# Kernel optimization log

Measured on AMD Instinct MI355X. Metric: run time of the kernel, lower is better.

The kernel has to match this reference:

```python
import jax, jax.numpy as jnp
import numpy as np

NB, B, IN, HID = 8, 256, 512, 512
G = 4 * HID
WB, IB, ABNM = 8, 8, 8
NL = 0.05


def quant(x, bits, r):
    # QuantFunc.forward: scale, clamp to (-1+1/step, 1-1/step), round to step grid, rescale
    step = 2.0 ** (bits - 1)
    x01 = jnp.clip(x / r, -1.0 + 1.0 / step, 1.0 - 1.0 / step)
    return jnp.round(x01 * step) / step * r


def pact(x, a):
    # pact_a_bmm vectorized over the block dim: sign(x)*0.5*(|x| - ||x|-a| + a)
    a3 = a[:, None, None]
    return jnp.sign(x) * 0.5 * (jnp.abs(x) - jnp.abs(jnp.abs(x) - a3) + a3)


def custom_mm(inp, w, b, nw, nb):
    # CustomMM_bmm.forward: quantize weights/bias (range 1.0), add scaled noise, bmm
    wq = quant(w, WB, 1.0)
    bq = quant(b, WB, 1.0)
    out = jnp.einsum('bni,bio->bno', inp, wq + nw * jnp.max(w) * NL)
    return out + bq + nb * jnp.max(b) * NL


def setup_inputs():
    key = jax.random.key(0)
    ks = jax.random.split(key, 11)
    inp = {
        'input': jax.random.normal(ks[0], (B, IN), jnp.float32),
        'hx': jax.random.normal(ks[1], (NB, B, HID), jnp.float32),
        'cx': jax.random.normal(ks[2], (NB, B, HID), jnp.float32),
        'weight_ih': jax.random.normal(ks[3], (NB, IN, G), jnp.float32),
        'weight_hh': jax.random.normal(ks[4], (NB, HID, G), jnp.float32),
        'bias_ih': jax.random.normal(ks[5], (NB, 1, G), jnp.float32),
        'bias_hh': jax.random.normal(ks[6], (NB, 1, G), jnp.float32),
        'noise_wih': jax.random.normal(ks[7], (NB, IN, G), jnp.float32),
        'noise_whh': jax.random.normal(ks[8], (NB, HID, G), jnp.float32),
        'noise_bih': jax.random.normal(ks[9], (NB, 1, G), jnp.float32),
        'noise_bhh': jax.random.normal(ks[10], (NB, 1, G), jnp.float32),
        'a1': jnp.full((NB,), 128.0, jnp.float32),
        'a3': jnp.ones((NB,), jnp.float32),
        'a4': jnp.ones((NB,), jnp.float32),
        'a5': jnp.ones((NB,), jnp.float32),
        'a6': jnp.ones((NB,), jnp.float32),
        'a7': jnp.full((NB,), 4.0, jnp.float32),
        'a8': jnp.ones((NB,), jnp.float32),
        'a9': jnp.full((NB,), 4.0, jnp.float32),
        'a10': jnp.ones((NB,), jnp.float32),
        'a11': jnp.full((NB,), 4.0, jnp.float32),
    }
    return inp


def reference(input, hx, cx, weight_ih, weight_hh, bias_ih, bias_hh,
              noise_wih, noise_whh, noise_bih, noise_bhh,
              a1, a3, a4, a5, a6, a7, a8, a9, a10, a11):
    xr = jnp.broadcast_to(input[None], (NB,) + input.shape)  # input.repeat(n_blocks,1,1)
    xq = quant(pact(xr, a1), IB, a1[:, None, None])
    gates = custom_mm(xq, weight_ih, bias_ih, noise_wih, noise_bih) \
          + custom_mm(hx, weight_hh, bias_hh, noise_whh, noise_bhh)
    i, j, f, o = jnp.split(gates, 4, axis=2)
    qp = lambda x, a: quant(pact(x, a), ABNM, a[:, None, None])
    fg = qp(jax.nn.sigmoid(f), a3)
    ig = qp(jax.nn.sigmoid(i), a4)
    act = qp(jnp.tanh(j), a5)
    og = qp(jax.nn.sigmoid(o), a6)
    gated = qp(cx * fg, a7)
    actin = qp(ig * act, a8)
    new_c = qp(gated + actin, a9)
    actc = qp(jnp.tanh(new_c), a10)
    new_h = qp(actc * og, a11)
    return new_h, new_c
```

## Files before the change

### kernel.cpp

```cpp
#include <hip/hip_runtime.h>
#include <hip/hip_bf16.h>

#define NBATCH 8
#define BROWS 256
#define KDIM 512
#define HIDD 512
#define GDIM 2048
#define KSTEP 32
#define NIT (KDIM / KSTEP)

typedef float f32x4 __attribute__((ext_vector_type(4)));
typedef __bf16 bf16x8 __attribute__((ext_vector_type(8)));

__device__ __forceinline__ unsigned fenc(float f) {
    unsigned u = __float_as_uint(f);
    return (u & 0x80000000u) ? ~u : (u | 0x80000000u);
}
__device__ __forceinline__ float fdec(unsigned e) {
    unsigned u = (e & 0x80000000u) ? (e & 0x7fffffffu) : ~e;
    return __uint_as_float(u);
}
__device__ __forceinline__ unsigned umaxu(unsigned a, unsigned b) { return a > b ? a : b; }

__device__ __forceinline__ float qpact(float x, float a) {
    float ax = fabsf(x);
    float p  = copysignf(0.5f * (ax - fabsf(ax - a) + a), x);
    float x01 = p / a;
    x01 = fminf(fmaxf(x01, -0.9921875f), 0.9921875f);
    return (rintf(x01 * 128.f) * 0.0078125f) * a;
}
__device__ __forceinline__ float q1(float x) {
    float x01 = fminf(fmaxf(x, -0.9921875f), 0.9921875f);
    return rintf(x01 * 128.f) * 0.0078125f;
}
__device__ __forceinline__ float sigmf(float x) { return 1.0f / (1.0f + expf(-x)); }

__global__ void k_init(unsigned* m) { if (threadIdx.x < 4) m[threadIdx.x] = 0u; }

__global__ void k_max(const float* __restrict__ w_ih, const float* __restrict__ w_hh,
                      const float* __restrict__ b_ih, const float* __restrict__ b_hh,
                      unsigned* __restrict__ omax) {
    int which = blockIdx.y;
    const float* src = which == 0 ? w_ih : which == 1 ? w_hh : which == 2 ? b_ih : b_hh;
    int n4 = (which < 2 ? NBATCH * KDIM * GDIM : NBATCH * GDIM) >> 2;
    unsigned best = 0u;
    int stride = gridDim.x * blockDim.x;
    for (int i = blockIdx.x * blockDim.x + threadIdx.x; i < n4; i += stride) {
        float4 v = ((const float4*)src)[i];
        best = umaxu(best, fenc(v.x)); best = umaxu(best, fenc(v.y));
        best = umaxu(best, fenc(v.z)); best = umaxu(best, fenc(v.w));
    }
    #pragma unroll
    for (int off = 32; off > 0; off >>= 1)
        best = umaxu(best, (unsigned)__shfl_down((int)best, off, 64));
    __shared__ unsigned red[4];
    int lane = threadIdx.x & 63, wv = threadIdx.x >> 6;
    if (lane == 0) red[wv] = best;
    __syncthreads();
    if (threadIdx.x == 0) {
        unsigned b2 = umaxu(umaxu(red[0], red[1]), umaxu(red[2], red[3]));
        atomicMax(&omax[which], b2);
    }
}

__global__ void k_prep(const float* __restrict__ input, const float* __restrict__ hx,
                       const float* __restrict__ bih, const float* __restrict__ bhh,
                       const float* __restrict__ nbih, const float* __restrict__ nbhh,
                       const float* __restrict__ a1, const unsigned* __restrict__ maxes,
                       __hip_bfloat16* __restrict__ xqh, __hip_bfloat16* __restrict__ hxh,
                       __hip_bfloat16* __restrict__ hxl, float* __restrict__ bias_comb) {
    const int NX = NBATCH * BROWS * KDIM;
    const int NH = NBATCH * BROWS * HIDD;
    const int NBC = NBATCH * GDIM;
    int total = NX + NH + NBC;
    int stride = gridDim.x * blockDim.x;
    for (int i = blockIdx.x * blockDim.x + threadIdx.x; i < total; i += stride) {
        if (i < NX) {
            int nb = i >> 17;
            int rem = i & 131071;
            float v = qpact(input[rem], a1[nb]);
            xqh[i] = __float2bfloat16(v);
        } else if (i < NX + NH) {
            int j = i - NX;
            float h = hx[j];
            __hip_bfloat16 hi = __float2bfloat16(h);
            hxh[j] = hi;
            hxl[j] = __float2bfloat16(h - __bfloat162float(hi));
        } else {
            int j = i - NX - NH;
            float mb_ih = fdec(maxes[2]);
            float mb_hh = fdec(maxes[3]);
            bias_comb[j] = q1(bih[j]) + (nbih[j] * mb_ih) * 0.05f
                         + q1(bhh[j]) + (nbhh[j] * mb_hh) * 0.05f;
        }
    }
}

__global__ __launch_bounds__(512, 2) void k_gemm(
    const float* __restrict__ w_ih, const float* __restrict__ w_hh,
    const float* __restrict__ n_ih, const float* __restrict__ n_hh,
    const __hip_bfloat16* __restrict__ xqh, const __hip_bfloat16* __restrict__ hxh,
    const __hip_bfloat16* __restrict__ hxl,
    const float* __restrict__ bias_comb, const float* __restrict__ cx,
    const float* __restrict__ a3, const float* __restrict__ a4, const float* __restrict__ a5,
    const float* __restrict__ a6, const float* __restrict__ a7, const float* __restrict__ a8,
    const float* __restrict__ a9, const float* __restrict__ a10, const float* __restrict__ a11,
    const unsigned* __restrict__ maxes,
    float* __restrict__ out_h, float* __restrict__ out_c)
{
    __shared__ __hip_bfloat16 Bsm[2][4][64][40];

    int tid = threadIdx.x;
    int lane = tid & 63, wv = tid >> 6;
    int nb = blockIdx.x & 7;
    int cb = blockIdx.x >> 3;

    const float* wih_b = w_ih + nb * KDIM * GDIM;
    const float* whh_b = w_hh + nb * KDIM * GDIM;
    const float* nih_b = n_ih + nb * KDIM * GDIM;
    const float* nhh_b = n_hh + nb * KDIM * GDIM;
    const __hip_bfloat16* xq_b = xqh + nb * BROWS * KDIM;
    const __hip_bfloat16* hh_b = hxh + nb * BROWS * KDIM;
    const __hip_bfloat16* hl_b = hxl + nb * BROWS * KDIM;

    float c_ih = fdec(maxes[0]);
    float c_hh = fdec(maxes[1]);

    f32x4 acc[2][4] = {};

    int lh = lane & 15;
    int lk = (lane >> 4) << 3;
    int m0 = wv << 5;

    int sn0 = (tid & 15) << 2;
    int sk  = tid >> 4;
    int scol = ((sn0 >> 4) << 9) + (cb << 4) + (sn0 & 15);
    int sbase = sk * GDIM + scol;

    f32x4 rw1a, rz1a, rw2a, rz2a;
    f32x4 rw1b, rz1b, rw2b, rz2b;
    bf16x8 axv[2], ahv[2], alv[2];

#define STAGE(RW1, RZ1, RW2, RZ2, K0) {            \
    int gx = sbase + (K0) * GDIM;                  \
    RW1 = *(const f32x4*)(wih_b + gx);             \
    RZ1 = *(const f32x4*)(nih_b + gx);             \
    RW2 = *(const f32x4*)(whh_b + gx);             \
    RZ2 = *(const f32x4*)(nhh_b + gx); }

#define ALOAD(K0) {                                \
    _Pragma("unroll")                              \
    for (int mf = 0; mf < 2; ++mf) {               \
        int aoff = (m0 + (mf << 4) + lh) * KDIM + (K0) + lk; \
        axv[mf] = *(const bf16x8*)(xq_b + aoff);   \
        ahv[mf] = *(const bf16x8*)(hh_b + aoff);   \
        alv[mf] = *(const bf16x8*)(hl_b + aoff); } }

#define CVT(P, RW1, RZ1, RW2, RZ2) {               \
    _Pragma("unroll")                              \
    for (int j = 0; j < 4; ++j) {                  \
        float w1 = RW1[j], z1 = RZ1[j];            \
        float wq1 = rintf(fminf(fmaxf(w1, -0.9921875f), 0.9921875f) * 128.f) * 0.0078125f; \
        float e1 = wq1 + (z1 * c_ih) * 0.05f;      \
        __hip_bfloat16 h1 = __float2bfloat16(e1);  \
        Bsm[P][0][sn0 + j][sk] = h1;               \
        Bsm[P][1][sn0 + j][sk] = __float2bfloat16(e1 - __bfloat162float(h1)); \
        float w2 = RW2[j], z2 = RZ2[j];            \
        float wq2 = rintf(fminf(fmaxf(w2, -0.9921875f), 0.9921875f) * 128.f) * 0.0078125f; \
        float e2 = wq2 + (z2 * c_hh) * 0.05f;      \
        __hip_bfloat16 h2 = __float2bfloat16(e2);  \
        Bsm[P][2][sn0 + j][sk] = h2;               \
        Bsm[P][3][sn0 + j][sk] = __float2bfloat16(e2 - __bfloat162float(h2)); \
    } }

#define COMPUTE(P) {                               \
    _Pragma("unroll")                              \
    for (int nf = 0; nf < 4; ++nf) {               \
        int n = (nf << 4) + lh;                    \
        bf16x8 b0 = *(const bf16x8*)&Bsm[P][0][n][lk]; \
        bf16x8 b1 = *(const bf16x8*)&Bsm[P][1][n][lk]; \
        bf16x8 b2 = *(const bf16x8*)&Bsm[P][2][n][lk]; \
        bf16x8 b3 = *(const bf16x8*)&Bsm[P][3][n][lk]; \
        _Pragma("unroll")                          \
        for (int mf = 0; mf < 2; ++mf) {           \
            acc[mf][nf] = __builtin_amdgcn_mfma_f32_16x16x32_bf16(axv[mf], b0, acc[mf][nf], 0, 0, 0); \
            acc[mf][nf] = __builtin_amdgcn_mfma_f32_16x16x32_bf16(axv[mf], b1, acc[mf][nf], 0, 0, 0); \
            acc[mf][nf] = __builtin_amdgcn_mfma_f32_16x16x32_bf16(ahv[mf], b2, acc[mf][nf], 0, 0, 0); \
            acc[mf][nf] = __builtin_amdgcn_mfma_f32_16x16x32_bf16(ahv[mf], b3, acc[mf][nf], 0, 0, 0); \
            acc[mf][nf] = __builtin_amdgcn_mfma_f32_16x16x32_bf16(alv[mf], b2, acc[mf][nf], 0, 0, 0); \
        } \
    } }

    STAGE(rw1a, rz1a, rw2a, rz2a, 0);
    STAGE(rw1b, rz1b, rw2b, rz2b, KSTEP);

    for (int it = 0; it < NIT; it += 2) {
        ALOAD(it * KSTEP);
        CVT(0, rw1a, rz1a, rw2a, rz2a);
        if (it + 2 < NIT) STAGE(rw1a, rz1a, rw2a, rz2a, (it + 2) * KSTEP);
        __syncthreads();
        COMPUTE(0);
        ALOAD((it + 1) * KSTEP);
        CVT(1, rw1b, rz1b, rw2b, rz2b);
        if (it + 3 < NIT) STAGE(rw1b, rz1b, rw2b, rz2b, (it + 3) * KSTEP);
        __syncthreads();
        COMPUTE(1);
    }

    int hcol = (cb << 4) + lh;
    float A3 = a3[nb], A4 = a4[nb], A5 = a5[nb], A6 = a6[nb], A7 = a7[nb];
    float A8 = a8[nb], A9 = a9[nb], A10 = a10[nb], A11 = a11[nb];
    float bc_i = bias_comb[nb * GDIM + hcol];
    float bc_j = bias_comb[nb * GDIM + 512 + hcol];
    float bc_f = bias_comb[nb * GDIM + 1024 + hcol];
    float bc_o = bias_comb[nb * GDIM + 1536 + hcol];
    #pragma unroll
    for (int mf = 0; mf < 2; ++mf)
        #pragma unroll
        for (int rg = 0; rg < 4; ++rg) {
            int r = m0 + (mf << 4) + ((lane >> 4) << 2) + rg;
            float gi = acc[mf][0][rg] + bc_i;
            float gj = acc[mf][1][rg] + bc_j;
            float gf = acc[mf][2][rg] + bc_f;
            float go = acc[mf][3][rg] + bc_o;
            float fg = qpact(sigmf(gf), A3);
            float ig = qpact(sigmf(gi), A4);
            float act = qpact(tanhf(gj), A5);
            float og = qpact(sigmf(go), A6);
            int oidx = (nb * BROWS + r) * HIDD + hcol;
            float cv = cx[oidx];
            float gated = qpact(cv * fg, A7);
            float actin = qpact(ig * act, A8);
            float ncv = qpact(gated + actin, A9);
            float acv = qpact(tanhf(ncv), A10);
            float nhv = qpact(acv * og, A11);
            out_h[oidx] = nhv;
            out_c[oidx] = ncv;
        }
}

extern "C" void kernel_launch(void* const* d_in, const int* in_sizes, int n_in,
                              void* d_out, int out_size, void* d_ws, size_t ws_size,
                              hipStream_t stream) {
    const float* input = (const float*)d_in[0];
    const float* hx    = (const float*)d_in[1];
    const float* cx    = (const float*)d_in[2];
    const float* w_ih  = (const float*)d_in[3];
    const float* w_hh  = (const float*)d_in[4];
    const float* b_ih  = (const float*)d_in[5];
    const float* b_hh  = (const float*)d_in[6];
    const float* n_wih = (const float*)d_in[7];
    const float* n_whh = (const float*)d_in[8];
    const float* n_bih = (const float*)d_in[9];
    const float* n_bhh = (const float*)d_in[10];
    const float* a1  = (const float*)d_in[11];
    const float* a3  = (const float*)d_in[12];
    const float* a4  = (const float*)d_in[13];
    const float* a5  = (const float*)d_in[14];
    const float* a6  = (const float*)d_in[15];
    const float* a7  = (const float*)d_in[16];
    const float* a8  = (const float*)d_in[17];
    const float* a9  = (const float*)d_in[18];
    const float* a10 = (const float*)d_in[19];
    const float* a11 = (const float*)d_in[20];

    float* out_h = (float*)d_out;
    float* out_c = out_h + NBATCH * BROWS * HIDD;

    char* ws = (char*)d_ws;
    unsigned* maxes = (unsigned*)ws;
    __hip_bfloat16* xqh = (__hip_bfloat16*)(ws + 256);
    __hip_bfloat16* hxh = (__hip_bfloat16*)(ws + 256 + 2097152);
    __hip_bfloat16* hxl = (__hip_bfloat16*)(ws + 256 + 2 * 2097152);
    float* bias_comb    = (float*)(ws + 256 + 3 * 2097152);

    k_init<<<1, 64, 0, stream>>>(maxes);
    k_max<<<dim3(256, 4), 256, 0, stream>>>(w_ih, w_hh, b_ih, b_hh, maxes);
    k_prep<<<2048, 256, 0, stream>>>(input, hx, b_ih, b_hh, n_bih, n_bhh, a1, maxes,
                                     xqh, hxh, hxl, bias_comb);
    k_gemm<<<NBATCH * 32, 512, 0, stream>>>(w_ih, w_hh, n_wih, n_whh, xqh, hxh, hxl,
                                            bias_comb, cx,
                                            a3, a4, a5, a6, a7, a8, a9, a10, a11,
                                            maxes, out_h, out_c);
}
```

Before: 80.19 us.

## Use 1024-thread blocks with 16-row warp tiles and 64-wide K steps

The GEMM block grows to 1024 threads (16 waves), each wave covering 16 rows instead of 32, and the K step doubles to 64 with a larger shared tile. Weight staging switches from float4 vector loads to scalar loads across four gate column groups, and A fragments are loaded directly inside the compute loop. The aim is more waves to hide the latency of the weight stream and fewer barriers per K. In exchange, each B tile in shared memory is reused by fewer rows per wave, global loads become scalar but still coalesced, and occupancy drops to one block per CU with tighter register limits.

```diff
diff --git a/kernel.cpp b/kernel.cpp
--- a/kernel.cpp
+++ b/kernel.cpp
@@ -6,7 +6,7 @@
 #define KDIM 512
 #define HIDD 512
 #define GDIM 2048
-#define KSTEP 32
+#define KSTEP 64
 #define NIT (KDIM / KSTEP)
 
 typedef float f32x4 __attribute__((ext_vector_type(4)));
@@ -96,7 +96,7 @@
     }
 }
 
-__global__ __launch_bounds__(512, 2) void k_gemm(
+__global__ __launch_bounds__(1024, 1) void k_gemm(
     const float* __restrict__ w_ih, const float* __restrict__ w_hh,
     const float* __restrict__ n_ih, const float* __restrict__ n_hh,
     const __hip_bfloat16* __restrict__ xqh, const __hip_bfloat16* __restrict__ hxh,
@@ -108,7 +108,7 @@
     const unsigned* __restrict__ maxes,
     float* __restrict__ out_h, float* __restrict__ out_c)
 {
-    __shared__ __hip_bfloat16 Bsm[2][4][64][40];
+    __shared__ __hip_bfloat16 Bsm[2][4][64][72];
 
     int tid = threadIdx.x;
     int lane = tid & 63, wv = tid >> 6;
@@ -126,68 +126,65 @@
     float c_ih = fdec(maxes[0]);
     float c_hh = fdec(maxes[1]);
 
-    f32x4 acc[2][4] = {};
+    f32x4 acc[4] = {};
 
     int lh = lane & 15;
-    int lk = (lane >> 4) << 3;
-    int m0 = wv << 5;
-
-    int sn0 = (tid & 15) << 2;
-    int sk  = tid >> 4;
-    int scol = ((sn0 >> 4) << 9) + (cb << 4) + (sn0 & 15);
-    int sbase = sk * GDIM + scol;
-
-    f32x4 rw1a, rz1a, rw2a, rz2a;
-    f32x4 rw1b, rz1b, rw2b, rz2b;
-    bf16x8 axv[2], ahv[2], alv[2];
-
-#define STAGE(RW1, RZ1, RW2, RZ2, K0) {            \
-    int gx = sbase + (K0) * GDIM;                  \
-    RW1 = *(const f32x4*)(wih_b + gx);             \
-    RZ1 = *(const f32x4*)(nih_b + gx);             \
-    RW2 = *(const f32x4*)(whh_b + gx);             \
-    RZ2 = *(const f32x4*)(nhh_b + gx); }
-
-#define ALOAD(K0) {                                \
-    _Pragma("unroll")                              \
-    for (int mf = 0; mf < 2; ++mf) {               \
-        int aoff = (m0 + (mf << 4) + lh) * KDIM + (K0) + lk; \
-        axv[mf] = *(const bf16x8*)(xq_b + aoff);   \
-        ahv[mf] = *(const bf16x8*)(hh_b + aoff);   \
-        alv[mf] = *(const bf16x8*)(hl_b + aoff); } }
-
-#define CVT(P, RW1, RZ1, RW2, RZ2) {               \
-    _Pragma("unroll")                              \
-    for (int j = 0; j < 4; ++j) {                  \
-        float w1 = RW1[j], z1 = RZ1[j];            \
+    int g  = lane >> 4;
+    int arow = (wv << 4) + lh;
+
+    int c  = tid & 15;
+    int kk = tid >> 4;
+
+    float rw1a[4], rz1a[4], rw2a[4], rz2a[4];
+    float rw1b[4], rz1b[4], rw2b[4], rz2b[4];
+
+#define STAGE(R1, Z1, R2, Z2, K0) {                          \
+    int base = ((K0) + kk) * GDIM + (cb << 4) + c;           \
+    _Pragma("unroll")                                        \
+    for (int nf = 0; nf < 4; ++nf) {                         \
+        int gx = base + (nf << 9);                           \
+        R1[nf] = wih_b[gx]; Z1[nf] = nih_b[gx];              \
+        R2[nf] = whh_b[gx]; Z2[nf] = nhh_b[gx];              \
+    } }
+
+#define CVT(P, R1, Z1, R2, Z2) {                             \
+    _Pragma("unroll")                                        \
+    for (int nf = 0; nf < 4; ++nf) {                         \
+        int n = (nf << 4) + c;                               \
+        float w1 = R1[nf], z1 = Z1[nf];                      \
         float wq1 = rintf(fminf(fmaxf(w1, -0.9921875f), 0.9921875f) * 128.f) * 0.0078125f; \
-        float e1 = wq1 + (z1 * c_ih) * 0.05f;      \
-        __hip_bfloat16 h1 = __float2bfloat16(e1);  \
-        Bsm[P][0][sn0 + j][sk] = h1;               \
-        Bsm[P][1][sn0 + j][sk] = __float2bfloat16(e1 - __bfloat162float(h1)); \
-        float w2 = RW2[j], z2 = RZ2[j];            \
+        float e1 = wq1 + (z1 * c_ih) * 0.05f;                \
+        __hip_bfloat16 h1 = __float2bfloat16(e1);            \
+        Bsm[P][0][n][kk] = h1;                               \
+        Bsm[P][1][n][kk] = __float2bfloat16(e1 - __bfloat162float(h1)); \
+        float w2 = R2[nf], z2 = Z2[nf];                      \
         float wq2 = rintf(fminf(fmaxf(w2, -0.9921875f), 0.9921875f) * 128.f) * 0.0078125f; \
-        float e2 = wq2 + (z2 * c_hh) * 0.05f;      \
-        __hip_bfloat16 h2 = __float2bfloat16(e2);  \
-        Bsm[P][2][sn0 + j][sk] = h2;               \
-        Bsm[P][3][sn0 + j][sk] = __float2bfloat16(e2 - __bfloat162float(h2)); \
+        float e2 = wq2 + (z2 * c_hh) * 0.05f;                \
+        __hip_bfloat16 h2 = __float2bfloat16(e2);            \
+        Bsm[P][2][n][kk] = h2;                               \
+        Bsm[P][3][n][kk] = __float2bfloat16(e2 - __bfloat162float(h2)); \
     } }
 
-#define COMPUTE(P) {                               \
-    _Pragma("unroll")                              \
-    for (int nf = 0; nf < 4; ++nf) {               \
-        int n = (nf << 4) + lh;                    \
-        bf16x8 b0 = *(const bf16x8*)&Bsm[P][0][n][lk]; \
-        bf16x8 b1 = *(const bf16x8*)&Bsm[P][1][n][lk]; \
-        bf16x8 b2 = *(const bf16x8*)&Bsm[P][2][n][lk]; \
-        bf16x8 b3 = *(const bf16x8*)&Bsm[P][3][n][lk]; \
-        _Pragma("unroll")                          \
-        for (int mf = 0; mf < 2; ++mf) {           \
-            acc[mf][nf] = __builtin_amdgcn_mfma_f32_16x16x32_bf16(axv[mf], b0, acc[mf][nf], 0, 0, 0); \
-            acc[mf][nf] = __builtin_amdgcn_mfma_f32_16x16x32_bf16(axv[mf], b1, acc[mf][nf], 0, 0, 0); \
-            acc[mf][nf] = __builtin_amdgcn_mfma_f32_16x16x32_bf16(ahv[mf], b2, acc[mf][nf], 0, 0, 0); \
-            acc[mf][nf] = __builtin_amdgcn_mfma_f32_16x16x32_bf16(ahv[mf], b3, acc[mf][nf], 0, 0, 0); \
-            acc[mf][nf] = __builtin_amdgcn_mfma_f32_16x16x32_bf16(alv[mf], b2, acc[mf][nf], 0, 0, 0); \
+#define COMPUTE(P, K0) {                                     \
+    _Pragma("unroll")                                        \
+    for (int kf = 0; kf < 2; ++kf) {                         \
+        int ko = (K0) + (kf << 5) + (g << 3);                \
+        int kb = (kf << 5) + (g << 3);                       \
+        bf16x8 ax = *(const bf16x8*)(xq_b + arow * KDIM + ko); \
+        bf16x8 ah = *(const bf16x8*)(hh_b + arow * KDIM + ko); \
+        bf16x8 al = *(const bf16x8*)(hl_b + arow * KDIM + ko); \
+        _Pragma("unroll")                                    \
+        for (int nf = 0; nf < 4; ++nf) {                     \
+            int n = (nf << 4) + lh;                          \
+            bf16x8 b0 = *(const bf16x8*)&Bsm[P][0][n][kb];   \
+            bf16x8 b1 = *(const bf16x8*)&Bsm[P][1][n][kb];   \
+            bf16x8 b2 = *(const bf16x8*)&Bsm[P][2][n][kb];   \
+            bf16x8 b3 = *(const bf16x8*)&Bsm[P][3][n][kb];   \
+            acc[nf] = __builtin_amdgcn_mfma_f32_16x16x32_bf16(ax, b0, acc[nf], 0, 0, 0); \
+            acc[nf] = __builtin_amdgcn_mfma_f32_16x16x32_bf16(ax, b1, acc[nf], 0, 0, 0); \
+            acc[nf] = __builtin_amdgcn_mfma_f32_16x16x32_bf16(ah, b2, acc[nf], 0, 0, 0); \
+            acc[nf] = __builtin_amdgcn_mfma_f32_16x16x32_bf16(ah, b3, acc[nf], 0, 0, 0); \
+            acc[nf] = __builtin_amdgcn_mfma_f32_16x16x32_bf16(al, b2, acc[nf], 0, 0, 0); \
         } \
     } }
 
@@ -195,16 +192,14 @@
     STAGE(rw1b, rz1b, rw2b, rz2b, KSTEP);
 
     for (int it = 0; it < NIT; it += 2) {
-        ALOAD(it * KSTEP);
         CVT(0, rw1a, rz1a, rw2a, rz2a);
         if (it + 2 < NIT) STAGE(rw1a, rz1a, rw2a, rz2a, (it + 2) * KSTEP);
         __syncthreads();
-        COMPUTE(0);
-        ALOAD((it + 1) * KSTEP);
+        COMPUTE(0, it * KSTEP);
         CVT(1, rw1b, rz1b, rw2b, rz2b);
         if (it + 3 < NIT) STAGE(rw1b, rz1b, rw2b, rz2b, (it + 3) * KSTEP);
         __syncthreads();
-        COMPUTE(1);
+        COMPUTE(1, (it + 1) * KSTEP);
     }
 
     int hcol = (cb << 4) + lh;
@@ -215,28 +210,26 @@
     float bc_f = bias_comb[nb * GDIM + 1024 + hcol];
     float bc_o = bias_comb[nb * GDIM + 1536 + hcol];
     #pragma unroll
-    for (int mf = 0; mf < 2; ++mf)
-        #pragma unroll
-        for (int rg = 0; rg < 4; ++rg) {
-            int r = m0 + (mf << 4) + ((lane >> 4) << 2) + rg;
-            float gi = acc[mf][0][rg] + bc_i;
-            float gj = acc[mf][1][rg] + bc_j;
-            float gf = acc[mf][2][rg] + bc_f;
-            float go = acc[mf][3][rg] + bc_o;
-            float fg = qpact(sigmf(gf), A3);
-            float ig = qpact(sigmf(gi), A4);
-            float act = qpact(tanhf(gj), A5);
-            float og = qpact(sigmf(go), A6);
-            int oidx = (nb * BROWS + r) * HIDD + hcol;
-            float cv = cx[oidx];
-            float gated = qpact(cv * fg, A7);
-            float actin = qpact(ig * act, A8);
-            float ncv = qpact(gated + actin, A9);
-            float acv = qpact(tanhf(ncv), A10);
-            float nhv = qpact(acv * og, A11);
-            out_h[oidx] = nhv;
-            out_c[oidx] = ncv;
-        }
+    for (int rg = 0; rg < 4; ++rg) {
+        int r = (wv << 4) + (g << 2) + rg;
+        float gi = acc[0][rg] + bc_i;
+        float gj = acc[1][rg] + bc_j;
+        float gf = acc[2][rg] + bc_f;
+        float go = acc[3][rg] + bc_o;
+        float fg = qpact(sigmf(gf), A3);
+        float ig = qpact(sigmf(gi), A4);
+        float act = qpact(tanhf(gj), A5);
+        float og = qpact(sigmf(go), A6);
+        int oidx = (nb * BROWS + r) * HIDD + hcol;
+        float cv = cx[oidx];
+        float gated = qpact(cv * fg, A7);
+        float actin = qpact(ig * act, A8);
+        float ncv = qpact(gated + actin, A9);
+        float acv = qpact(tanhf(ncv), A10);
+        float nhv = qpact(acv * og, A11);
+        out_h[oidx] = nhv;
+        out_c[oidx] = ncv;
+    }
 }
 
 extern "C" void kernel_launch(void* const* d_in, const int* in_sizes, int n_in,
@@ -278,8 +271,8 @@
     k_max<<<dim3(256, 4), 256, 0, stream>>>(w_ih, w_hh, b_ih, b_hh, maxes);
     k_prep<<<2048, 256, 0, stream>>>(input, hx, b_ih, b_hh, n_bih, n_bhh, a1, maxes,
                                      xqh, hxh, hxl, bias_comb);
-    k_gemm<<<NBATCH * 32, 512, 0, stream>>>(w_ih, w_hh, n_wih, n_whh, xqh, hxh, hxl,
-                                            bias_comb, cx,
-                                            a3, a4, a5, a6, a7, a8, a9, a10, a11,
-                                            maxes, out_h, out_c);
-}
+    k_gemm<<<NBATCH * 32, 1024, 0, stream>>>(w_ih, w_hh, n_wih, n_whh, xqh, hxh, hxl,
+                                             bias_comb, cx,
+                                             a3, a4, a5, a6, a7, a8, a9, a10, a11,
+                                             maxes, out_h, out_c);
+}
```

Result: slower. 85.15 us (+6.2%).
